# Optimization experiments

Measured on AMD Instinct MI355X. Metric: run time of the kernel, lower is better.

The kernel has to match this reference:

```python
import jax, jax.numpy as jnp
import numpy as np

B, L = 4, 8192
IN_CH, OUT_CH = 1, 1
H = 64               # d_model
NSTATE = 16          # d_state
DBLK = 4             # number of residual blocks
DCONV = 16
EXPAND = 2
DINNER = EXPAND * H              # 128
HEADDIM = H // 4                 # 16
NHEADS = DINNER // HEADDIM       # 8
CONV_DIM = DINNER + 2 * NSTATE   # 160 (ngroups=1)
D_IN_PROJ = 2 * DINNER + 2 * NSTATE + NHEADS  # 296
CHUNK = 128


def setup_inputs():
    key = jax.random.key(0)
    ks = jax.random.split(key, 12)
    rn = lambda k, shape, s: (jax.random.normal(k, shape) * s).astype(jnp.float32)
    x = rn(ks[0], (B, L, IN_CH), 1.0)
    w_in = rn(ks[1], (H, IN_CH), 1.0)
    w_out = rn(ks[2], (OUT_CH, H), 1.0 / np.sqrt(H))
    in_proj_w = rn(ks[3], (DBLK, D_IN_PROJ, H), 1.0 / np.sqrt(H))
    conv_w = rn(ks[4], (DBLK, CONV_DIM, DCONV), 1.0 / np.sqrt(DCONV))
    conv_b = rn(ks[5], (DBLK, CONV_DIM), 0.02)
    dt = jnp.exp(jax.random.uniform(ks[6], (DBLK, NHEADS)) * (np.log(0.1) - np.log(1e-3)) + np.log(1e-3))
    dt_bias = (dt + jnp.log(-jnp.expm1(-dt))).astype(jnp.float32)  # inverse softplus
    A_log = jnp.log(jax.random.uniform(ks[7], (DBLK, NHEADS), minval=1.0, maxval=16.0)).astype(jnp.float32)
    D_skip = jnp.ones((DBLK, NHEADS), jnp.float32)
    init_states = rn(ks[8], (DBLK, NHEADS, HEADDIM, NSTATE), 0.01)
    norm_w = jnp.ones((DBLK, DINNER), jnp.float32)
    out_proj_w = rn(ks[9], (DBLK, H, DINNER), 1.0 / np.sqrt(DINNER))
    mlp_w = rn(ks[10], (DBLK, H, H), 1.0 / np.sqrt(H))
    mlp_b = jnp.zeros((DBLK, H), jnp.float32)
    return {"x": x, "w_in": w_in, "w_out": w_out, "in_proj_w": in_proj_w,
            "conv_w": conv_w, "conv_b": conv_b, "dt_bias": dt_bias, "A_log": A_log,
            "D_skip": D_skip, "init_states": init_states, "norm_w": norm_w,
            "out_proj_w": out_proj_w, "mlp_w": mlp_w, "mlp_b": mlp_b}


def segsum(a):
    # a: (..., q) -> (..., q, q); seg[i, j] = sum_{k=j+1..i} a[k] on lower triangle (diag=0), exp->0 above
    q = a.shape[-1]
    cs = jnp.cumsum(a, axis=-1)
    seg = cs[..., :, None] - cs[..., None, :]
    mask = jnp.tril(jnp.ones((q, q), dtype=bool))
    return jnp.where(mask, seg, -1e30)


def ssd(X, dA, Bm, Cm, init_state):
    # Chunked SSD (Mamba2 paper). X: (b,l,h,p) = x*dt, dA: (b,l,h), Bm/Cm: (b,l,n), init_state: (b,h,p,n)
    b, l, h, p = X.shape
    c = l // CHUNK
    X = X.reshape(b, c, CHUNK, h, p)
    Bm = Bm.reshape(b, c, CHUNK, NSTATE)
    Cm = Cm.reshape(b, c, CHUNK, NSTATE)
    A = dA.reshape(b, c, CHUNK, h).transpose(0, 3, 1, 2)  # (b,h,c,q)
    A_cs = jnp.cumsum(A, axis=-1)
    # intra-chunk (diagonal blocks)
    Lm = jnp.exp(segsum(A))  # (b,h,c,q,q)
    Y_diag = jnp.einsum('bcln,bcsn,bhcls,bcshp->bclhp', Cm, Bm, Lm, X)
    # per-chunk final states
    decay_states = jnp.exp(A_cs[..., -1:] - A_cs)  # (b,h,c,q)
    states = jnp.einsum('bcln,bhcl,bclhp->bchpn', Bm, decay_states, X)
    states = jnp.concatenate([init_state[:, None], states], axis=1)  # (b,c+1,h,p,n)
    # inter-chunk recurrence (vectorized via segsum over chunk decays)
    decay_chunk = jnp.exp(segsum(jnp.pad(A_cs[..., -1], ((0, 0), (0, 0), (1, 0)))))  # (b,h,c+1,c+1)
    new_states = jnp.einsum('bhzc,bchpn->bzhpn', decay_chunk, states)
    prev_states = new_states[:, :-1]  # state entering each chunk
    state_decay = jnp.exp(A_cs)
    Y_off = jnp.einsum('bcln,bchpn,bhcl->bclhp', Cm, prev_states, state_decay)
    return (Y_diag + Y_off).reshape(b, l, h, p)


def mamba2(u, w_inp, cw, cb, dtb, alog, dskip, istate, nw, w_outp):
    b, l, _ = u.shape
    zxbcdt = jnp.einsum('bld,ed->ble', u, w_inp)  # (b,l,296)
    z = zxbcdt[..., :DINNER]
    xBC = zxbcdt[..., DINNER:DINNER + CONV_DIM]
    dt = jax.nn.softplus(zxbcdt[..., DINNER + CONV_DIM:] + dtb)  # (b,l,h)
    # causal depthwise conv over seq + silu
    xBC = jax.lax.conv_general_dilated(
        xBC.transpose(0, 2, 1), cw[:, None, :], (1,), [(DCONV - 1, 0)],
        feature_group_count=CONV_DIM, dimension_numbers=('NCH', 'OIH', 'NCH'))
    xBC = jax.nn.silu(xBC + cb[None, :, None]).transpose(0, 2, 1)
    xs = xBC[..., :DINNER]
    Bm = xBC[..., DINNER:DINNER + NSTATE]
    Cm = xBC[..., DINNER + NSTATE:]
    A = -jnp.exp(alog)  # (h,)
    xh = xs.reshape(b, l, NHEADS, HEADDIM)
    init = jnp.broadcast_to(istate, (b,) + istate.shape)
    y = ssd(xh * dt[..., None], dt * A, Bm, Cm, init)
    y = y + xh * dskip[None, None, :, None]  # D skip
    y = y.reshape(b, l, DINNER)
    # gated RMSNorm: norm(y * silu(z)) * weight
    y = y * jax.nn.silu(z)
    y = y * jax.lax.rsqrt(jnp.mean(y * y, axis=-1, keepdims=True) + 1e-5) * nw
    return jnp.einsum('ble,de->bld', y, w_outp)


def reference(x, w_in, w_out, in_proj_w, conv_w, conv_b, dt_bias, A_log,
              D_skip, init_states, norm_w, out_proj_w, mlp_w, mlp_b):
    h = jnp.einsum('bli,hi->blh', x, w_in)
    for i in range(DBLK):
        y = mamba2(h, in_proj_w[i], conv_w[i], conv_b[i], dt_bias[i], A_log[i],
                   D_skip[i], init_states[i], norm_w[i], out_proj_w[i])
        t = y / jnp.sqrt(1.0 + y * y)  # TanhApprox
        y = jnp.einsum('blh,oh->blo', t, mlp_w[i]) + mlp_b[i]
        h = h + y  # residual
    return jnp.einsum('blh,oh->blo', h, w_out)
```

## Files before the change

kernel.cpp:

```cpp
#include <hip/hip_runtime.h>
#include <math.h>

#define NB 4
#define SEQ 8192
#define NT (NB*SEQ)
#define HDIM 64
#define NST 16
#define NBLK 4
#define KCONV 16
#define DIN 128
#define PDIM 16
#define NH 8
#define CDIM 160
#define EPROJ 296
#define CH 128
#define NC 64

typedef __attribute__((ext_vector_type(8))) short short8;
typedef __attribute__((ext_vector_type(4))) float f32x4;

__device__ __forceinline__ float sigf(float x){ return 1.0f/(1.0f+__expf(-x)); }

__device__ __forceinline__ unsigned short bf16r(float f){
  unsigned int u = __float_as_uint(f);
  u = (u + 0x7fffu + ((u >> 16) & 1u)) >> 16;
  return (unsigned short)u;
}
__device__ __forceinline__ unsigned int pk_bf16(float a, float b){
  return (unsigned int)bf16r(a) | ((unsigned int)bf16r(b) << 16);
}
__device__ __forceinline__ float bf16f(unsigned short h){
  return __uint_as_float(((unsigned int)h) << 16);
}

__global__ __launch_bounds__(256) void k_init_h(const float* __restrict__ x, const float* __restrict__ w_in,
                                                float* __restrict__ h){
  int i = blockIdx.x*256 + threadIdx.x;
  int t = i >> 6, d = i & 63;
  h[i] = x[t]*w_in[d];
}

__global__ __launch_bounds__(256) void k_wsplit(const float* __restrict__ w,
                                                unsigned short* __restrict__ whi,
                                                unsigned short* __restrict__ wlo){
  int i = blockIdx.x*256 + threadIdx.x;
  if(i < NBLK*EPROJ*HDIM){
    float f = w[i];
    unsigned short hi = bf16r(f);
    float fh = bf16f(hi);
    whi[i] = hi;
    wlo[i] = bf16r(f - fh);
  }
}

__global__ __launch_bounds__(256) void k_inproj(const float* __restrict__ h,
                                                const unsigned short* __restrict__ whi,
                                                const unsigned short* __restrict__ wlo,
                                                unsigned short* __restrict__ zxz,
                                                float* __restrict__ zxc){
  int tid = threadIdx.x;
  int lane = tid & 63, wid = tid >> 6;
  int quad = lane >> 4, lq = lane & 15;
  int t0 = blockIdx.x*64 + wid*16;

  const float* hp = h + (size_t)(t0+lq)*HDIM;
  short8 bh[2], bl[2];
#pragma unroll
  for(int kb=0;kb<2;kb++){
    float4 f0 = *(const float4*)(hp + kb*32 + quad*8);
    float4 f1 = *(const float4*)(hp + kb*32 + quad*8 + 4);
    float v[8] = {f0.x,f0.y,f0.z,f0.w,f1.x,f1.y,f1.z,f1.w};
#pragma unroll
    for(int j=0;j<8;j++){
      unsigned short hi = bf16r(v[j]);
      bh[kb][j] = (short)hi;
      bl[kb][j] = (short)bf16r(v[j] - bf16f(hi));
    }
  }

  for(int et=0; et<19; et++){
    int e_a = et*16 + lq;
    int ec = (e_a < EPROJ) ? e_a : (EPROJ-1);
    const unsigned short* wh = whi + (size_t)ec*HDIM + quad*8;
    const unsigned short* wl = wlo + (size_t)ec*HDIM + quad*8;
    short8 ah0 = *(const short8*)wh;
    short8 ah1 = *(const short8*)(wh + 32);
    short8 al0 = *(const short8*)wl;
    short8 al1 = *(const short8*)(wl + 32);
    f32x4 acc = {0.f,0.f,0.f,0.f};
    acc = __builtin_amdgcn_mfma_f32_16x16x32_bf16(ah0, bh[0], acc, 0, 0, 0);
    acc = __builtin_amdgcn_mfma_f32_16x16x32_bf16(ah1, bh[1], acc, 0, 0, 0);
    acc = __builtin_amdgcn_mfma_f32_16x16x32_bf16(ah0, bl[0], acc, 0, 0, 0);
    acc = __builtin_amdgcn_mfma_f32_16x16x32_bf16(ah1, bl[1], acc, 0, 0, 0);
    acc = __builtin_amdgcn_mfma_f32_16x16x32_bf16(al0, bh[0], acc, 0, 0, 0);
    acc = __builtin_amdgcn_mfma_f32_16x16x32_bf16(al1, bh[1], acc, 0, 0, 0);
#pragma unroll
    for(int r=0;r<4;r++){
      int e = et*16 + quad*4 + r;
      if(e < 128)        zxz[(size_t)e*NT + t0 + lq] = bf16r(acc[r]);
      else if(e < EPROJ) zxc[(size_t)(e-128)*NT + t0 + lq] = acc[r];
    }
  }
}

__global__ __launch_bounds__(512) void k_mid(const float* __restrict__ zxc,
                                             const float* __restrict__ cw, const float* __restrict__ cb,
                                             const float* __restrict__ dtb, const float* __restrict__ alog,
                                             unsigned short* __restrict__ xbc, float* __restrict__ dt,
                                             float* __restrict__ acs, float* __restrict__ asum,
                                             float* __restrict__ S){
  __shared__ unsigned short XhT[128][136];
  __shared__ unsigned short XlT[128][136];
  __shared__ unsigned short BhT[16][136];
  __shared__ unsigned short BlT[16][136];
  __shared__ float dtl[8][128];
  __shared__ float wle[8][128];

  int bc = blockIdx.x;
  int c = bc & 63, b = bc >> 6;
  int t0 = b*SEQ + c*CH;
  int tid = threadIdx.x;

  for(int it=0; it<5; it++){
    int G = tid + it*512;
    int ch = G >> 4;
    int sg = (G & 15) * 8;
    const float* p = zxc + (size_t)ch*NT + t0 + sg - 16;
    float buf[24];
    if(c == 0 && sg < 16){
#pragma unroll
      for(int j=0;j<24;j++){
        int l = sg - 16 + j;
        buf[j] = (l >= 0) ? p[j] : 0.f;
      }
    } else {
#pragma unroll
      for(int q4=0;q4<6;q4++){
        float4 f = *(const float4*)(p + q4*4);
        buf[q4*4+0]=f.x; buf[q4*4+1]=f.y; buf[q4*4+2]=f.z; buf[q4*4+3]=f.w;
      }
    }
    float wv[16];
#pragma unroll
    for(int k=0;k<16;k++) wv[k] = cw[ch*KCONV+k];
    float bias = cb[ch];
    unsigned short hs[8];
#pragma unroll
    for(int s=0;s<8;s++){
      float acc = bias;
#pragma unroll
      for(int k=0;k<16;k++) acc += wv[k]*buf[s+1+k];
      float r = acc * sigf(acc);
      unsigned short hi = bf16r(r);
      unsigned short lo = bf16r(r - bf16f(hi));
      hs[s] = hi;
      if(ch < 128){ XhT[ch][sg+s] = hi; XlT[ch][sg+s] = lo; }
      else if(ch < 144){ BhT[ch-128][sg+s] = hi; BlT[ch-128][sg+s] = lo; }
    }
    uint4 pk;
    pk.x = (unsigned int)hs[0] | ((unsigned int)hs[1] << 16);
    pk.y = (unsigned int)hs[2] | ((unsigned int)hs[3] << 16);
    pk.z = (unsigned int)hs[4] | ((unsigned int)hs[5] << 16);
    pk.w = (unsigned int)hs[6] | ((unsigned int)hs[7] << 16);
    *(uint4*)(xbc + (size_t)ch*NT + t0 + sg) = pk;
  }
#pragma unroll
  for(int k=0;k<2;k++){
    int idx = tid + k*512;
    int hh = idx >> 7, s = idx & 127;
    float raw = zxc[(size_t)(CDIM + hh)*NT + t0 + s] + dtb[hh];
    float v = (raw > 20.f) ? raw : log1pf(__expf(raw));
    dtl[hh][s] = v;
    dt[(size_t)hh*NT + t0 + s] = v;
  }
  __syncthreads();

  int lane = tid & 63, wid = tid >> 6;
  {
    int hh = wid;
    float A = -__expf(alog[hh]);
    float d0 = dtl[hh][2*lane], d1 = dtl[hh][2*lane+1];
    float v0 = d0*A, v1 = d1*A;
    float s = v0 + v1;
    for(int off=1; off<64; off<<=1){
      float o = __shfl_up(s, off);
      if(lane >= off) s += o;
    }
    float tot = __shfl(s, 63);
    float excl = s - (v0+v1);
    float a0 = excl+v0, a1 = excl+v0+v1;
    *(float2*)&acs[(size_t)hh*NT + t0 + 2*lane] = make_float2(a0, a1);
    if(lane == 63) asum[(size_t)bc*NH + hh] = tot;
    wle[hh][2*lane]   = d0*__expf(tot - a0);
    wle[hh][2*lane+1] = d1*__expf(tot - a1);
  }
  __syncthreads();

  {
    int hh = wid;
    int lq = lane & 15, quad = lane >> 4;
    f32x4 acc = {0.f,0.f,0.f,0.f};
#pragma unroll
    for(int kb=0;kb<4;kb++){
      int k0 = kb*32 + quad*8;
      short8 xh = *(const short8*)&XhT[hh*16 + lq][k0];
      short8 xl = *(const short8*)&XlT[hh*16 + lq][k0];
      short8 ah, al;
#pragma unroll
      for(int j=0;j<8;j++){
        float xv = bf16f((unsigned short)xh[j]) + bf16f((unsigned short)xl[j]);
        float pw = xv * wle[hh][k0 + j];
        unsigned short hi = bf16r(pw);
        ah[j] = (short)hi;
        al[j] = (short)bf16r(pw - bf16f(hi));
      }
      short8 bh = *(const short8*)&BhT[lq][k0];
      short8 bl = *(const short8*)&BlT[lq][k0];
      acc = __builtin_amdgcn_mfma_f32_16x16x32_bf16(ah, bh, acc, 0, 0, 0);
      acc = __builtin_amdgcn_mfma_f32_16x16x32_bf16(ah, bl, acc, 0, 0, 0);
      acc = __builtin_amdgcn_mfma_f32_16x16x32_bf16(al, bh, acc, 0, 0, 0);
    }
    float* Sp = S + ((size_t)bc*NH + hh)*256;
#pragma unroll
    for(int r=0;r<4;r++) Sp[(quad*4 + r)*16 + lq] = acc[r];
  }
}

__global__ __launch_bounds__(64) void k_scan(const float* __restrict__ S, const float* __restrict__ asum,
                                             const float* __restrict__ init, float* __restrict__ prev){
  int q  = blockIdx.x & 3;
  int hh = (blockIdx.x >> 2) & 7;
  int b  = blockIdx.x >> 5;
  int el = q*64 + threadIdx.x;
  const size_t cs = (size_t)NH*256;
  const float* Sp = S + ((size_t)(b*NC)*NH + hh)*256 + el;
  float* Pp = prev + ((size_t)(b*NC)*NH + hh)*256 + el;
  const float* ap = asum + (size_t)(b*NC)*NH + hh;
  float r = init[hh*256 + el];
  float s0 = Sp[0], s1 = Sp[cs], s2 = Sp[2*cs], s3 = Sp[3*cs];
  for(int c=0;c<NC;c+=4){
    Pp[(size_t)c*cs] = r;
    r = __expf(ap[(size_t)c*NH])*r + s0;
    s0 = (c+4 < NC) ? Sp[(size_t)(c+4)*cs] : 0.f;
    Pp[(size_t)(c+1)*cs] = r;
    r = __expf(ap[(size_t)(c+1)*NH])*r + s1;
    s1 = (c+5 < NC) ? Sp[(size_t)(c+5)*cs] : 0.f;
    Pp[(size_t)(c+2)*cs] = r;
    r = __expf(ap[(size_t)(c+2)*NH])*r + s2;
    s2 = (c+6 < NC) ? Sp[(size_t)(c+6)*cs] : 0.f;
    Pp[(size_t)(c+3)*cs] = r;
    r = __expf(ap[(size_t)(c+3)*NH])*r + s3;
    s3 = (c+7 < NC) ? Sp[(size_t)(c+7)*cs] : 0.f;
  }
}

__global__ __launch_bounds__(512) void k_tail(const unsigned short* __restrict__ xbc,
                                              const unsigned short* __restrict__ zxz,
                                              const float* __restrict__ dt, const float* __restrict__ acs,
                                              const float* __restrict__ prev, const float* __restrict__ dskip,
                                              const float* __restrict__ nw, const float* __restrict__ opw,
                                              const float* __restrict__ mw, const float* __restrict__ mb,
                                              float* __restrict__ h,
                                              int last, const float* __restrict__ wout,
                                              float* __restrict__ out){
  __shared__ __align__(16) unsigned char sm[142336];
  unsigned short* Bb   = (unsigned short*)(sm);
  unsigned short* Cb   = (unsigned short*)(sm + 6144);
  unsigned short* XbT  = (unsigned short*)(sm + 12288);
  unsigned short* Sraw = (unsigned short*)(sm + 55296);
  unsigned short* P    = (unsigned short*)(sm + 90112);
  float* Al  = (float*)(sm + 133120);
  float* Dtl = (float*)(sm + 137216);
  float* nwl = (float*)(sm + 141312);
  float* mbl = (float*)(sm + 141824);
  unsigned short* zbuf = (unsigned short*)(sm + 142080);
  unsigned short* Wo = Sraw;
  unsigned short* Wm = Sraw + 64*136;
  unsigned short* Zb = XbT;
  unsigned short* Yn = P;
  unsigned short* Tt = P;

  int bc = blockIdx.x;
  int c = bc & 63, b = bc >> 6;
  int t0 = b*SEQ + c*CH;
  int tid = threadIdx.x, lane = tid & 63, wid = tid >> 6;
  int quad = lane >> 4, lq = lane & 15;

#pragma unroll
  for(int k=0;k<8;k++){
    int idx = tid + k*512;
    int ch = idx >> 7, s = idx & 127;
    unsigned short f = xbc[(size_t)(DIN+ch)*NT + t0 + s];
    if(ch < 16) Bb[s*24 + ch] = f;
    else        Cb[s*24 + ch-16] = f;
  }
#pragma unroll
  for(int k=0;k<8;k++){
    int fi = tid + k*512;
    int p = fi >> 5, s4 = fi & 31;
    uint2 xu = *(const uint2*)&xbc[(size_t)p*NT + t0 + s4*4];
    float4 dv = *(const float4*)&dt[(size_t)(p>>4)*NT + t0 + s4*4];
    float x0 = bf16f((unsigned short)(xu.x & 0xffffu));
    float x1 = bf16f((unsigned short)(xu.x >> 16));
    float x2 = bf16f((unsigned short)(xu.y & 0xffffu));
    float x3 = bf16f((unsigned short)(xu.y >> 16));
    *(unsigned int*)&XbT[p*168 + s4*4]   = pk_bf16(x0*dv.x, x1*dv.y);
    *(unsigned int*)&XbT[p*168 + s4*4+2] = pk_bf16(x2*dv.z, x3*dv.w);
  }
#pragma unroll
  for(int k=0;k<4;k++){
    int idx = tid + k*512;
    int hh = idx >> 8, rest = idx & 255;
    int p = rest >> 4, n = rest & 15;
    XbT[(hh*16+p)*168 + 128 + n] = bf16r(prev[((size_t)bc*NH + hh)*256 + rest]);
  }
#pragma unroll
  for(int k=0;k<3;k++){
    int idx = tid + k*512;
    int p = idx / 12, cc = idx - p*12;
    *(unsigned int*)&XbT[p*168 + 144 + 2*cc] = 0u;
  }
#pragma unroll
  for(int k=0;k<2;k++){
    int idx = tid + k*512;
    int hh = idx >> 7, s = idx & 127;
    Al[hh*128+s]  = acs[(size_t)hh*NT + t0 + s];
    Dtl[hh*128+s] = dt[(size_t)hh*NT + t0 + s];
  }
  if(tid < 128) nwl[tid] = nw[tid];
  else if(tid < 192) mbl[tid-128] = mb[tid-128];
  else if(tid < 208) zbuf[tid-192] = 0;
  __syncthreads();

  int strip = wid*16;
  short8 afr;
  {
    int row = strip + lq;
    const unsigned short* ap = (quad < 2) ? &Cb[row*24 + quad*8] : zbuf;
    afr = *(const short8*)ap;
  }
  for(int nt=0;nt<8;nt++){
    const unsigned short* bp = (quad < 2) ? &Bb[(nt*16+lq)*24 + quad*8] : zbuf;
    short8 bfr = *(const short8*)bp;
    f32x4 acc = {0.f,0.f,0.f,0.f};
    acc = __builtin_amdgcn_mfma_f32_16x16x32_bf16(afr, bfr, acc, 0, 0, 0);
#pragma unroll
    for(int r=0;r<4;r++)
      Sraw[(strip+quad*4+r)*136 + nt*16+lq] = bf16r(acc[r]);
  }

  f32x4 accv[8];
  int c0 = 2*lane, c1 = 2*lane+1;
  for(int hh2=0; hh2<8; hh2++){
    const float* Alh = Al + hh2*128;
    const float* Dth = Dtl + hh2*128;
    float as0 = Alh[c0], as1 = Alh[c1];
#pragma unroll
    for(int rr=0;rr<16;rr++){
      int row = strip + rr;
      float alr = Alh[row];
      unsigned int sv = *(unsigned int*)&Sraw[row*136 + c0];
      float s0 = bf16f((unsigned short)(sv & 0xffffu));
      float s1 = bf16f((unsigned short)(sv >> 16));
      float p0 = s0 * __expf(alr - as0);
      float p1 = s1 * __expf(alr - as1);
      p0 = (c0 <= row) ? p0 : 0.f;
      p1 = (c1 <= row) ? p1 : 0.f;
      *(unsigned int*)&P[row*168 + c0] = pk_bf16(p0, p1);
    }
    {
      int n = lane & 15, rg = lane >> 4;
#pragma unroll
      for(int rr=0;rr<4;rr++){
        int row = strip + rg*4 + rr;
        float ea = __expf(Alh[row]);
        P[row*168 + 128 + n] = bf16r(bf16f(Cb[row*24+n]) * ea);
      }
    }
    {
      int cc = lane & 7, rg = lane >> 3;
#pragma unroll
      for(int rr=0;rr<2;rr++){
        int row = strip + rg*2 + rr;
        *(unsigned int*)&P[row*168 + 144 + 2*cc] = 0u;
      }
    }
    f32x4 acc2 = {0.f,0.f,0.f,0.f};
#pragma unroll
    for(int ks=0;ks<5;ks++){
      short8 bfr = *(const short8*)&XbT[(hh2*16+lq)*168 + ks*32 + quad*8];
      short8 af  = *(const short8*)&P[(strip+lq)*168 + ks*32 + quad*8];
      acc2 = __builtin_amdgcn_mfma_f32_16x16x32_bf16(af, bfr, acc2, 0, 0, 0);
    }
    float Dk = dskip[hh2];
#pragma unroll
    for(int r=0;r<4;r++){
      int l = strip + quad*4 + r;
      float xdt = bf16f(XbT[(hh2*16+lq)*168 + l]);
      float dtv = fmaxf(Dth[l], 1e-30f);
      acc2[r] += Dk * xdt * __frcp_rn(dtv);
    }
    accv[hh2] = acc2;
  }
  __syncthreads();

#pragma unroll
  for(int k=0;k<8;k++){
    int fi = tid + k*512;
    int p = fi >> 5, s4 = fi & 31;
    uint2 zu = *(const uint2*)&zxz[(size_t)p*NT + t0 + s4*4];
    *(unsigned int*)&Zb[p*136 + s4*4]   = zu.x;
    *(unsigned int*)&Zb[p*136 + s4*4+2] = zu.y;
  }
#pragma unroll
  for(int k=0;k<4;k++){
    int fi = tid + k*512;
    int n = fi >> 5, k4 = fi & 31;
    float4 wv = *(const float4*)&opw[(size_t)n*DIN + k4*4];
    *(unsigned int*)&Wo[n*136 + k4*4]   = pk_bf16(wv.x, wv.y);
    *(unsigned int*)&Wo[n*136 + k4*4+2] = pk_bf16(wv.z, wv.w);
  }
#pragma unroll
  for(int k=0;k<2;k++){
    int fi = tid + k*512;
    int n = fi >> 4, k4 = fi & 15;
    float4 wv = *(const float4*)&mw[(size_t)n*HDIM + k4*4];
    *(unsigned int*)&Wm[n*72 + k4*4]   = pk_bf16(wv.x, wv.y);
    *(unsigned int*)&Wm[n*72 + k4*4+2] = pk_bf16(wv.z, wv.w);
  }
  __syncthreads();

  float rms_[4];
#pragma unroll
  for(int r=0;r<4;r++){
    int l = strip + quad*4 + r;
    float part = 0.f;
#pragma unroll
    for(int hh2=0;hh2<8;hh2++){
      float zv = bf16f(Zb[(hh2*16+lq)*136 + l]);
      float g = zv * sigf(zv);
      float yv = accv[hh2][r] * g;
      accv[hh2][r] = yv;
      part += yv*yv;
    }
    part += __shfl_xor(part,1); part += __shfl_xor(part,2);
    part += __shfl_xor(part,4); part += __shfl_xor(part,8);
    rms_[r] = rsqrtf(part*(1.0f/128.0f) + 1e-5f);
  }
#pragma unroll
  for(int hh2=0;hh2<8;hh2++){
    float nwv = nwl[hh2*16+lq];
#pragma unroll
    for(int r=0;r<4;r++){
      int l = strip + quad*4 + r;
      Yn[l*136 + hh2*16+lq] = bf16r(accv[hh2][r]*rms_[r]*nwv);
    }
  }

  short8 afk[4];
#pragma unroll
  for(int ks=0;ks<4;ks++) afk[ks] = *(const short8*)&Yn[(strip+lq)*136 + ks*32 + quad*8];
  f32x4 aco[4];
#pragma unroll
  for(int nt=0;nt<4;nt++){ aco[nt] = (f32x4){0.f,0.f,0.f,0.f}; }
#pragma unroll
  for(int nt=0;nt<4;nt++){
#pragma unroll
    for(int ks=0;ks<4;ks++){
      short8 bfr = *(const short8*)&Wo[(nt*16+lq)*136 + ks*32 + quad*8];
      aco[nt] = __builtin_amdgcn_mfma_f32_16x16x32_bf16(afk[ks], bfr, aco[nt], 0, 0, 0);
    }
  }

#pragma unroll
  for(int nt=0;nt<4;nt++){
#pragma unroll
    for(int r=0;r<4;r++){
      int l = strip + quad*4 + r;
      float o = aco[nt][r];
      Tt[l*136 + nt*16+lq] = bf16r(o * rsqrtf(1.0f + o*o));
    }
  }

  f32x4 acm[4];
#pragma unroll
  for(int nt=0;nt<4;nt++){ acm[nt] = (f32x4){0.f,0.f,0.f,0.f}; }
#pragma unroll
  for(int ks=0;ks<2;ks++){
    short8 af = *(const short8*)&Tt[(strip+lq)*136 + ks*32 + quad*8];
#pragma unroll
    for(int nt=0;nt<4;nt++){
      short8 bfr = *(const short8*)&Wm[(nt*16+lq)*72 + ks*32 + quad*8];
      acm[nt] = __builtin_amdgcn_mfma_f32_16x16x32_bf16(af, bfr, acm[nt], 0, 0, 0);
    }
  }
  if(!last){
#pragma unroll
    for(int nt=0;nt<4;nt++){
#pragma unroll
      for(int r=0;r<4;r++){
        int l = strip + quad*4 + r;
        int d = nt*16 + lq;
        size_t gi = (size_t)(t0+l)*HDIM + d;
        h[gi] += acm[nt][r] + mbl[d];
      }
    }
  } else {
    float ps[4] = {0.f,0.f,0.f,0.f};
#pragma unroll
    for(int nt=0;nt<4;nt++){
      int d = nt*16 + lq;
      float wo = wout[d];
      float bias = mbl[d];
#pragma unroll
      for(int r=0;r<4;r++){
        int l = strip + quad*4 + r;
        size_t gi = (size_t)(t0+l)*HDIM + d;
        float hn = h[gi] + acm[nt][r] + bias;
        ps[r] += hn * wo;
      }
    }
#pragma unroll
    for(int r=0;r<4;r++){
      ps[r] += __shfl_xor(ps[r],1); ps[r] += __shfl_xor(ps[r],2);
      ps[r] += __shfl_xor(ps[r],4); ps[r] += __shfl_xor(ps[r],8);
    }
    if(lq == 0){
#pragma unroll
      for(int r=0;r<4;r++) out[t0 + strip + quad*4 + r] = ps[r];
    }
  }
}

extern "C" void kernel_launch(void* const* d_in, const int* in_sizes, int n_in,
                              void* d_out, int out_size, void* d_ws, size_t ws_size,
                              hipStream_t stream){
  const float* x          = (const float*)d_in[0];
  const float* w_in       = (const float*)d_in[1];
  const float* w_out      = (const float*)d_in[2];
  const float* in_proj_w  = (const float*)d_in[3];
  const float* conv_w     = (const float*)d_in[4];
  const float* conv_b     = (const float*)d_in[5];
  const float* dt_bias    = (const float*)d_in[6];
  const float* A_log      = (const float*)d_in[7];
  const float* D_skip     = (const float*)d_in[8];
  const float* init_st    = (const float*)d_in[9];
  const float* norm_w     = (const float*)d_in[10];
  const float* out_proj_w = (const float*)d_in[11];
  const float* mlp_w      = (const float*)d_in[12];
  const float* mlp_b      = (const float*)d_in[13];
  float* out = (float*)d_out;

  float* ws = (float*)d_ws;
  float* h    = ws; ws += (size_t)NT*HDIM;
  unsigned short* zxz = (unsigned short*)ws; ws += (size_t)(128*NT)/2;
  float* zxc  = ws; ws += (size_t)168*NT;
  unsigned short* xbc = (unsigned short*)ws; ws += (size_t)(CDIM*NT)/2;
  float* dt   = ws; ws += (size_t)NH*NT;
  float* acs  = ws; ws += (size_t)NH*NT;
  float* asum = ws; ws += (size_t)NB*NC*NH;
  float* S    = ws; ws += (size_t)NB*NC*NH*256;
  float* prev = ws; ws += (size_t)NB*NC*NH*256;
  unsigned short* whi = (unsigned short*)ws; ws += (size_t)(NBLK*EPROJ*HDIM)/2;
  unsigned short* wlo = (unsigned short*)ws; ws += (size_t)(NBLK*EPROJ*HDIM)/2;

  k_init_h<<<(NT*HDIM)/256, 256, 0, stream>>>(x, w_in, h);
  k_wsplit<<<(NBLK*EPROJ*HDIM + 255)/256, 256, 0, stream>>>(in_proj_w, whi, wlo);
  for(int i=0;i<NBLK;i++){
    k_inproj<<<NT/64, 256, 0, stream>>>(h, whi + (size_t)i*EPROJ*HDIM,
                                        wlo + (size_t)i*EPROJ*HDIM, zxz, zxc);
    k_mid   <<<NB*NC, 512, 0, stream>>>(zxc, conv_w + i*CDIM*KCONV, conv_b + i*CDIM,
                                        dt_bias + i*NH, A_log + i*NH,
                                        xbc, dt, acs, asum, S);
    k_scan  <<<NB*NH*4, 64, 0, stream>>>(S, asum, init_st + i*NH*256, prev);
    k_tail  <<<NB*NC, 512, 0, stream>>>(xbc, zxz, dt, acs, prev, D_skip + i*NH,
                                        norm_w + i*DIN, out_proj_w + i*HDIM*DIN,
                                        mlp_w + i*HDIM*HDIM, mlp_b + i*HDIM, h,
                                        (i == NBLK-1) ? 1 : 0, w_out, out);
  }
}
```

Before: 379.3 us.

## Keep CB scores in registers and double-buffer decay-masked P per head

The C·B^T score tiles stay in MFMA accumulator registers instead of being written to a bf16 LDS buffer. The decay-weighted masked P tile is now built straight from those registers, in the MFMA output layout. P is double-buffered, so the tile for head h+1 is written while the MFMA for head h runs, and the zero padding columns are set once up front. This removes the Sraw round trip and the bf16 rounding of the scores, at the cost of more registers and extra LDS that may lower occupancy.

Result: faster. 370.3 us (-2.4%).

```diff
diff --git a/kernel.cpp b/kernel.cpp
--- a/kernel.cpp
+++ b/kernel.cpp
@@ -263,22 +263,22 @@
                                               float* __restrict__ h,
                                               int last, const float* __restrict__ wout,
                                               float* __restrict__ out){
-  __shared__ __align__(16) unsigned char sm[142336];
+  __shared__ __align__(16) unsigned char sm[150304];
   unsigned short* Bb   = (unsigned short*)(sm);
   unsigned short* Cb   = (unsigned short*)(sm + 6144);
   unsigned short* XbT  = (unsigned short*)(sm + 12288);
-  unsigned short* Sraw = (unsigned short*)(sm + 55296);
-  unsigned short* P    = (unsigned short*)(sm + 90112);
-  float* Al  = (float*)(sm + 133120);
-  float* Dtl = (float*)(sm + 137216);
-  float* nwl = (float*)(sm + 141312);
-  float* mbl = (float*)(sm + 141824);
-  unsigned short* zbuf = (unsigned short*)(sm + 142080);
-  unsigned short* Wo = Sraw;
-  unsigned short* Wm = Sraw + 64*136;
+  unsigned short* P0   = (unsigned short*)(sm + 55296);
+  unsigned short* P1   = (unsigned short*)(sm + 98304);
+  float* Al  = (float*)(sm + 141312);
+  float* Dtl = (float*)(sm + 145408);
+  float* nwl = (float*)(sm + 149504);
+  float* mbl = (float*)(sm + 150016);
+  unsigned short* zbuf = (unsigned short*)(sm + 150272);
   unsigned short* Zb = XbT;
-  unsigned short* Yn = P;
-  unsigned short* Tt = P;
+  unsigned short* Wo = P0;
+  unsigned short* Wm = P0 + 64*136;
+  unsigned short* Yn = P1;
+  unsigned short* Tt = P1;
 
   int bc = blockIdx.x;
   int c = bc & 63, b = bc >> 6;
@@ -333,65 +333,92 @@
   __syncthreads();
 
   int strip = wid*16;
+#pragma unroll
+  for(int k=0;k<3;k++){
+    int idx = lane + k*64;
+    int rr = idx / 12, cc = idx - rr*12;
+    *(unsigned int*)&P0[(strip+rr)*168 + 144 + 2*cc] = 0u;
+    *(unsigned int*)&P1[(strip+rr)*168 + 144 + 2*cc] = 0u;
+  }
+
   short8 afr;
   {
     int row = strip + lq;
     const unsigned short* ap = (quad < 2) ? &Cb[row*24 + quad*8] : zbuf;
     afr = *(const short8*)ap;
   }
+  f32x4 sc[8];
+#pragma unroll
   for(int nt=0;nt<8;nt++){
     const unsigned short* bp = (quad < 2) ? &Bb[(nt*16+lq)*24 + quad*8] : zbuf;
     short8 bfr = *(const short8*)bp;
     f32x4 acc = {0.f,0.f,0.f,0.f};
-    acc = __builtin_amdgcn_mfma_f32_16x16x32_bf16(afr, bfr, acc, 0, 0, 0);
-#pragma unroll
-    for(int r=0;r<4;r++)
-      Sraw[(strip+quad*4+r)*136 + nt*16+lq] = bf16r(acc[r]);
+    sc[nt] = __builtin_amdgcn_mfma_f32_16x16x32_bf16(afr, bfr, acc, 0, 0, 0);
   }
 
   f32x4 accv[8];
-  int c0 = 2*lane, c1 = 2*lane+1;
+  {
+    const float* Alh = Al;
+    unsigned short* Pb = P0;
+    float alr[4];
+#pragma unroll
+    for(int r=0;r<4;r++) alr[r] = Alh[strip + quad*4 + r];
+#pragma unroll
+    for(int nt=0;nt<8;nt++){
+      int col = nt*16 + lq;
+      float alc = Alh[col];
+#pragma unroll
+      for(int r=0;r<4;r++){
+        int row = strip + quad*4 + r;
+        float p = sc[nt][r] * __expf(alr[r] - alc);
+        p = (col <= row) ? p : 0.f;
+        Pb[row*168 + col] = bf16r(p);
+      }
+    }
+    int n = lane & 15, rg = lane >> 4;
+#pragma unroll
+    for(int rr=0;rr<4;rr++){
+      int row = strip + rg*4 + rr;
+      float ea = __expf(Alh[row]);
+      Pb[row*168 + 128 + n] = bf16r(bf16f(Cb[row*24+n]) * ea);
+    }
+  }
   for(int hh2=0; hh2<8; hh2++){
-    const float* Alh = Al + hh2*128;
-    const float* Dth = Dtl + hh2*128;
-    float as0 = Alh[c0], as1 = Alh[c1];
-#pragma unroll
-    for(int rr=0;rr<16;rr++){
-      int row = strip + rr;
-      float alr = Alh[row];
-      unsigned int sv = *(unsigned int*)&Sraw[row*136 + c0];
-      float s0 = bf16f((unsigned short)(sv & 0xffffu));
-      float s1 = bf16f((unsigned short)(sv >> 16));
-      float p0 = s0 * __expf(alr - as0);
-      float p1 = s1 * __expf(alr - as1);
-      p0 = (c0 <= row) ? p0 : 0.f;
-      p1 = (c1 <= row) ? p1 : 0.f;
-      *(unsigned int*)&P[row*168 + c0] = pk_bf16(p0, p1);
-    }
-    {
+    if(hh2 < 7){
+      const float* Alh = Al + (hh2+1)*128;
+      unsigned short* Pb = ((hh2+1)&1) ? P1 : P0;
+      float alr[4];
+#pragma unroll
+      for(int r=0;r<4;r++) alr[r] = Alh[strip + quad*4 + r];
+#pragma unroll
+      for(int nt=0;nt<8;nt++){
+        int col = nt*16 + lq;
+        float alc = Alh[col];
+#pragma unroll
+        for(int r=0;r<4;r++){
+          int row = strip + quad*4 + r;
+          float p = sc[nt][r] * __expf(alr[r] - alc);
+          p = (col <= row) ? p : 0.f;
+          Pb[row*168 + col] = bf16r(p);
+        }
+      }
       int n = lane & 15, rg = lane >> 4;
 #pragma unroll
       for(int rr=0;rr<4;rr++){
         int row = strip + rg*4 + rr;
         float ea = __expf(Alh[row]);
-        P[row*168 + 128 + n] = bf16r(bf16f(Cb[row*24+n]) * ea);
-      }
-    }
-    {
-      int cc = lane & 7, rg = lane >> 3;
-#pragma unroll
-      for(int rr=0;rr<2;rr++){
-        int row = strip + rg*2 + rr;
-        *(unsigned int*)&P[row*168 + 144 + 2*cc] = 0u;
-      }
-    }
+        Pb[row*168 + 128 + n] = bf16r(bf16f(Cb[row*24+n]) * ea);
+      }
+    }
+    const unsigned short* Pb = (hh2&1) ? P1 : P0;
     f32x4 acc2 = {0.f,0.f,0.f,0.f};
 #pragma unroll
     for(int ks=0;ks<5;ks++){
       short8 bfr = *(const short8*)&XbT[(hh2*16+lq)*168 + ks*32 + quad*8];
-      short8 af  = *(const short8*)&P[(strip+lq)*168 + ks*32 + quad*8];
+      short8 af  = *(const short8*)&Pb[(strip+lq)*168 + ks*32 + quad*8];
       acc2 = __builtin_amdgcn_mfma_f32_16x16x32_bf16(af, bfr, acc2, 0, 0, 0);
     }
+    const float* Dth = Dtl + hh2*128;
     float Dk = dskip[hh2];
 #pragma unroll
     for(int r=0;r<4;r++){
```
